# Kernel tuning notes

Hardware: AMD Instinct MI355X
Metric: run time of the kernel (lower is better)

## Reference

```python
import jax, jax.numpy as jnp
import numpy as np

B, D, S = 8192, 1024, 32  # batch, feature dim, number of sessions (experts)


def setup_inputs() -> dict:
    key = jax.random.key(0)
    k1, k2, k3, k4 = jax.random.split(key, 4)
    x = jax.random.normal(k1, (B, D), dtype=jnp.float32)
    # Expert bank: original init is identity affine; perturb so the test is nontrivial.
    W = jnp.eye(D, dtype=jnp.float32)[None, :, :] + 0.02 * jax.random.normal(k2, (S, D, D), dtype=jnp.float32)
    b = 0.02 * jax.random.normal(k3, (S, D), dtype=jnp.float32)
    session_idx = jax.random.randint(k4, (B,), 0, S)  # int session id per sample
    return {"x": x, "W": W, "b": b, "session_idx": session_idx}


def reference(x, W, b, session_idx):
    """Per-sample session-affine dispatch: out[i] = W[session_idx[i]] @ x[i] + b[session_idx[i]].

    Implemented as a scan over the (small, fixed) set of S experts: one dense
    [B,D]x[D,D] GEMM per expert, masked-accumulated into the output. This avoids
    gathering a [B,D,D] per-sample weight tensor.
    """
    num_sessions = W.shape[0]

    def step(acc, packed):
        Ws, bs, s = packed                       # Ws: [D,D], bs: [D]
        y = x @ Ws.T + bs                        # [B,D] dense affine for expert s
        mask = (session_idx == s)[:, None]       # [B,1] samples belonging to s
        return acc + jnp.where(mask, y, jnp.zeros((), x.dtype)), None

    out, _ = jax.lax.scan(step, jnp.zeros_like(x), (W, b, jnp.arange(num_sessions)))
    return out
```

## Files before the change

### kernel.cpp

```cpp
#include <hip/hip_runtime.h>
#include <cstddef>

#define B_ROWS 8192
#define DIM    1024
#define NSESS  32
#define MT     128
#define NTILE  128
#define BK     64
#define KITERS (DIM / BK)
#define TPE    3
#define LROW   72
#define TSZ    (MT * LROW)
#define NXCD   8
#define EPX    (NSESS / NXCD)
#define BPE    (TPE * (DIM / NTILE))

typedef __attribute__((ext_vector_type(8))) short short8;
typedef __attribute__((ext_vector_type(4))) float floatx4;
typedef __attribute__((ext_vector_type(4))) int intx4;
typedef __attribute__((ext_vector_type(2))) unsigned int uintx2;

__device__ __forceinline__ unsigned pack_bf16_2(float fa, float fb) {
  unsigned a = __builtin_bit_cast(unsigned, fa);
  unsigned b = __builtin_bit_cast(unsigned, fb);
  a += 0x7fffu + ((a >> 16) & 1u);
  b += 0x7fffu + ((b >> 16) & 1u);
  return __builtin_amdgcn_perm(b, a, 0x07060302u);
}

__global__ __launch_bounds__(256, 2) void gemm_kernel(
    const float* __restrict__ x, const float* __restrict__ W,
    const float* __restrict__ bias, const int* __restrict__ sidx,
    float* __restrict__ out)
{
  __shared__ __align__(16) short As0[TSZ], As1[TSZ];
  __shared__ __align__(16) short Bs0[TSZ], Bs1[TSZ];
  __shared__ int row_ids[MT];
  __shared__ int psum[256];

  const int hw    = blockIdx.x;
  const int xcd   = hw & (NXCD - 1);
  const int r     = hw >> 3;
  const int s     = xcd * EPX + (r / BPE);
  const int rr    = r % BPE;
  const int ntile = rr / TPE;
  const int mtile = rr % TPE;
  const int tid   = threadIdx.x;

  const intx4* sv = (const intx4*)(sidx + tid * 32);
  int c = 0;
#pragma unroll
  for (int j = 0; j < 8; ++j) {
    const intx4 v = sv[j];
#pragma unroll
    for (int e = 0; e < 4; ++e) c += (v[e] == s);
  }
  psum[tid] = c;
  __syncthreads();
#pragma unroll
  for (int d = 1; d < 256; d <<= 1) {
    const int mine = psum[tid];
    const int add  = (tid >= d) ? psum[tid - d] : 0;
    __syncthreads();
    psum[tid] = mine + add;
    __syncthreads();
  }
  const int total = psum[255];
  const int nrows = (total - mtile * MT) < 0 ? 0
                  : ((total - mtile * MT) > MT ? MT : (total - mtile * MT));
  if (nrows == 0) return;
  const int base_rank = psum[tid] - c;

  if (tid < MT) row_ids[tid] = -1;
  __syncthreads();
  {
    int r2 = base_rank;
    const int lo = mtile * MT, hi = lo + MT;
#pragma unroll
    for (int j = 0; j < 8; ++j) {
      const intx4 v = sv[j];
#pragma unroll
      for (int e = 0; e < 4; ++e) {
        if (v[e] == s) {
          if (r2 >= lo && r2 < hi) row_ids[r2 - lo] = tid * 32 + 4 * j + e;
          ++r2;
        }
      }
    }
  }
  __syncthreads();

  const int lane = tid & 63;
  const int wv   = tid >> 6;
  const int wm   = wv >> 1;
  const int wn   = wv & 1;
  const int fr   = lane & 15;
  const int kg   = lane >> 4;

  const int srow   = wv * 32 + (lane >> 4);
  const int schunk = lane & 15;

  const float* apt[8];
  const float* bpt[8];
#pragma unroll
  for (int j = 0; j < 8; ++j) {
    const int tr = srow + j * 4;
    int ar = row_ids[tr];
    if (ar < 0) ar = 0;
    apt[j] = x + (size_t)ar * DIM + schunk * 4;
    bpt[j] = W + (size_t)s * DIM * DIM + (size_t)(ntile * NTILE + tr) * DIM + schunk * 4;
  }

  floatx4 xreg[8], wreg[8];
  floatx4 acc[4][4] = {};

#define LOADREGS(KB)                                                           \
  {                                                                            \
    _Pragma("unroll")                                                          \
    for (int j = 0; j < 8; ++j) {                                              \
      xreg[j] = *(const floatx4*)(apt[j] + (KB) * BK);                         \
      wreg[j] = *(const floatx4*)(bpt[j] + (KB) * BK);                         \
    }                                                                          \
  }

#define CVTWRITE(AS, BS)                                                       \
  {                                                                            \
    _Pragma("unroll")                                                          \
    for (int j = 0; j < 8; ++j) {                                              \
      const int off = (srow + j * 4) * LROW + schunk * 4;                      \
      uintx2 ua = { pack_bf16_2(xreg[j][0], xreg[j][1]),                       \
                    pack_bf16_2(xreg[j][2], xreg[j][3]) };                     \
      uintx2 ub = { pack_bf16_2(wreg[j][0], wreg[j][1]),                       \
                    pack_bf16_2(wreg[j][2], wreg[j][3]) };                     \
      *(uintx2*)&AS[off] = ua;                                                 \
      *(uintx2*)&BS[off] = ub;                                                 \
    }                                                                          \
  }

#define COMPUTE(AS, BS)                                                        \
  {                                                                            \
    _Pragma("unroll")                                                          \
    for (int s2 = 0; s2 < 2; ++s2) {                                           \
      short8 fa[4], fb[4];                                                     \
      _Pragma("unroll")                                                        \
      for (int i = 0; i < 4; ++i) {                                            \
        fa[i] = *(const short8*)&AS[(wm * 64 + i * 16 + fr) * LROW + s2 * 32 + kg * 8]; \
        fb[i] = *(const short8*)&BS[(wn * 64 + i * 16 + fr) * LROW + s2 * 32 + kg * 8]; \
      }                                                                        \
      _Pragma("unroll")                                                        \
      for (int mi = 0; mi < 4; ++mi)                                           \
        _Pragma("unroll")                                                      \
        for (int ni = 0; ni < 4; ++ni)                                         \
          acc[mi][ni] = __builtin_amdgcn_mfma_f32_16x16x32_bf16(               \
              fa[mi], fb[ni], acc[mi][ni], 0, 0, 0);                           \
    }                                                                          \
  }

  LOADREGS(0);
  CVTWRITE(As0, Bs0);
  __syncthreads();

  for (int kb = 0; kb < KITERS; kb += 2) {
    LOADREGS(kb + 1);
    COMPUTE(As0, Bs0);
    CVTWRITE(As1, Bs1);
    __syncthreads();

    if (kb + 2 < KITERS) LOADREGS(kb + 2);
    COMPUTE(As1, Bs1);
    if (kb + 2 < KITERS) CVTWRITE(As0, Bs0);
    __syncthreads();
  }

#undef LOADREGS
#undef CVTWRITE
#undef COMPUTE

  const int col0 = ntile * NTILE + wn * 64;
#pragma unroll
  for (int ni = 0; ni < 4; ++ni) {
    const int n = col0 + ni * 16 + fr;
    const float bv = bias[s * DIM + n];
#pragma unroll
    for (int mi = 0; mi < 4; ++mi) {
      const int mbase = wm * 64 + mi * 16 + kg * 4;
#pragma unroll
      for (int rr2 = 0; rr2 < 4; ++rr2) {
        const int ml = mbase + rr2;
        if (ml < nrows) {
          const int orow = row_ids[ml];
          out[(size_t)orow * DIM + n] = acc[mi][ni][rr2] + bv;
        }
      }
    }
  }
}

extern "C" void kernel_launch(void* const* d_in, const int* in_sizes, int n_in,
                              void* d_out, int out_size, void* d_ws, size_t ws_size,
                              hipStream_t stream) {
  const float* x    = (const float*)d_in[0];
  const float* W    = (const float*)d_in[1];
  const float* b    = (const float*)d_in[2];
  const int*   sidx = (const int*)d_in[3];
  float* out = (float*)d_out;
  (void)d_ws; (void)ws_size;

  hipLaunchKernelGGL(gemm_kernel, dim3(NSESS * TPE * (DIM / NTILE)), dim3(256), 0, stream,
                     x, W, b, sidx, out);
}
```

Baseline: 289.2 us.

## Single-buffer LDS tiles, raise occupancy to 4 blocks, prefetch W before scan

```diff
diff --git a/kernel.cpp b/kernel.cpp
--- a/kernel.cpp
+++ b/kernel.cpp
@@ -28,13 +28,12 @@
   return __builtin_amdgcn_perm(b, a, 0x07060302u);
 }
 
-__global__ __launch_bounds__(256, 2) void gemm_kernel(
+__global__ __launch_bounds__(256, 4) void gemm_kernel(
     const float* __restrict__ x, const float* __restrict__ W,
     const float* __restrict__ bias, const int* __restrict__ sidx,
     float* __restrict__ out)
 {
-  __shared__ __align__(16) short As0[TSZ], As1[TSZ];
-  __shared__ __align__(16) short Bs0[TSZ], Bs1[TSZ];
+  __shared__ __align__(16) short As[TSZ], Bs[TSZ];
   __shared__ int row_ids[MT];
   __shared__ int psum[256];
 
@@ -47,6 +46,25 @@
   const int mtile = rr % TPE;
   const int tid   = threadIdx.x;
 
+  const int lane = tid & 63;
+  const int wv   = tid >> 6;
+  const int wm   = wv >> 1;
+  const int wn   = wv & 1;
+  const int fr   = lane & 15;
+  const int kg   = lane >> 4;
+
+  const int srow   = wv * 32 + (lane >> 4);
+  const int schunk = lane & 15;
+
+  const float* bpt[8];
+  floatx4 wreg[8];
+#pragma unroll
+  for (int j = 0; j < 8; ++j) {
+    const int tr = srow + j * 4;
+    bpt[j] = W + (size_t)s * DIM * DIM + (size_t)(ntile * NTILE + tr) * DIM + schunk * 4;
+    wreg[j] = *(const floatx4*)bpt[j];
+  }
+
   const intx4* sv = (const intx4*)(sidx + tid * 32);
   int c = 0;
 #pragma unroll
@@ -90,28 +108,17 @@
   }
   __syncthreads();
 
-  const int lane = tid & 63;
-  const int wv   = tid >> 6;
-  const int wm   = wv >> 1;
-  const int wn   = wv & 1;
-  const int fr   = lane & 15;
-  const int kg   = lane >> 4;
-
-  const int srow   = wv * 32 + (lane >> 4);
-  const int schunk = lane & 15;
-
   const float* apt[8];
-  const float* bpt[8];
+  floatx4 xreg[8];
 #pragma unroll
   for (int j = 0; j < 8; ++j) {
     const int tr = srow + j * 4;
     int ar = row_ids[tr];
     if (ar < 0) ar = 0;
     apt[j] = x + (size_t)ar * DIM + schunk * 4;
-    bpt[j] = W + (size_t)s * DIM * DIM + (size_t)(ntile * NTILE + tr) * DIM + schunk * 4;
-  }
-
-  floatx4 xreg[8], wreg[8];
+    xreg[j] = *(const floatx4*)apt[j];
+  }
+
   floatx4 acc[4][4] = {};
 
 #define LOADREGS(KB)                                                           \
@@ -123,7 +130,7 @@
     }                                                                          \
   }
 
-#define CVTWRITE(AS, BS)                                                       \
+#define CVTWRITE()                                                             \
   {                                                                            \
     _Pragma("unroll")                                                          \
     for (int j = 0; j < 8; ++j) {                                              \
@@ -132,20 +139,20 @@
                     pack_bf16_2(xreg[j][2], xreg[j][3]) };                     \
       uintx2 ub = { pack_bf16_2(wreg[j][0], wreg[j][1]),                       \
                     pack_bf16_2(wreg[j][2], wreg[j][3]) };                     \
-      *(uintx2*)&AS[off] = ua;                                                 \
-      *(uintx2*)&BS[off] = ub;                                                 \
+      *(uintx2*)&As[off] = ua;                                                 \
+      *(uintx2*)&Bs[off] = ub;                                                 \
     }                                                                          \
   }
 
-#define COMPUTE(AS, BS)                                                        \
+#define COMPUTE()                                                              \
   {                                                                            \
     _Pragma("unroll")                                                          \
     for (int s2 = 0; s2 < 2; ++s2) {                                           \
       short8 fa[4], fb[4];                                                     \
       _Pragma("unroll")                                                        \
       for (int i = 0; i < 4; ++i) {                                            \
-        fa[i] = *(const short8*)&AS[(wm * 64 + i * 16 + fr) * LROW + s2 * 32 + kg * 8]; \
-        fb[i] = *(const short8*)&BS[(wn * 64 + i * 16 + fr) * LROW + s2 * 32 + kg * 8]; \
+        fa[i] = *(const short8*)&As[(wm * 64 + i * 16 + fr) * LROW + s2 * 32 + kg * 8]; \
+        fb[i] = *(const short8*)&Bs[(wn * 64 + i * 16 + fr) * LROW + s2 * 32 + kg * 8]; \
       }                                                                        \
       _Pragma("unroll")                                                        \
       for (int mi = 0; mi < 4; ++mi)                                           \
@@ -156,20 +163,17 @@
     }                                                                          \
   }
 
-  LOADREGS(0);
-  CVTWRITE(As0, Bs0);
-  __syncthreads();
-
-  for (int kb = 0; kb < KITERS; kb += 2) {
-    LOADREGS(kb + 1);
-    COMPUTE(As0, Bs0);
-    CVTWRITE(As1, Bs1);
-    __syncthreads();
-
-    if (kb + 2 < KITERS) LOADREGS(kb + 2);
-    COMPUTE(As1, Bs1);
-    if (kb + 2 < KITERS) CVTWRITE(As0, Bs0);
-    __syncthreads();
+  CVTWRITE();
+  __syncthreads();
+
+  for (int kb = 0; kb < KITERS; ++kb) {
+    if (kb + 1 < KITERS) LOADREGS(kb + 1);
+    COMPUTE();
+    if (kb + 1 < KITERS) {
+      __syncthreads();
+      CVTWRITE();
+      __syncthreads();
+    }
   }
 
 #undef LOADREGS
```

New measurement: 379.9 us. 31.4% more time.
